# Kernel tuning notes

Hardware: AMD Instinct MI355X
Metric: run time of the kernel (lower is better)

Reference implementation:

```python
import jax, jax.numpy as jnp
import numpy as np

DIM = 4096
N_HEADS = 32
N_KV_HEADS = 8
HEAD_DIM = 128
ROPE_BASE = 10000.0
B, L = 4, 1024
NEG_INF = -1e9


def rope_traditional(x, base=ROPE_BASE, offset=0):
    # x: [B, H, L, Dh]; rotates interleaved pairs (x[...,2i], x[...,2i+1])
    Dh = x.shape[-1]
    Lx = x.shape[2]
    inv_freq = base ** (-jnp.arange(0, Dh, 2, dtype=jnp.float32) / Dh)  # [Dh/2]
    pos = jnp.arange(offset, offset + Lx, dtype=jnp.float32)
    ang = pos[:, None] * inv_freq  # [L, Dh/2]
    cos, sin = jnp.cos(ang), jnp.sin(ang)
    x1, x2 = x[..., ::2], x[..., 1::2]
    r1 = x1 * cos - x2 * sin
    r2 = x1 * sin + x2 * cos
    return jnp.stack([r1, r2], axis=-1).reshape(x.shape).astype(x.dtype)


def setup_inputs() -> dict:
    key = jax.random.key(0)
    ks = jax.random.split(key, 5)
    x = jax.random.normal(ks[0], (B, L, DIM), dtype=jnp.float32)
    # additive causal mask: 0 on/below diag, -inf-like above
    mask = jnp.where(jnp.tril(jnp.ones((L, L), dtype=bool)), 0.0, NEG_INF).astype(jnp.float32)
    wq = jax.random.normal(ks[1], (DIM, N_HEADS * HEAD_DIM), dtype=jnp.float32) * 0.02
    wk = jax.random.normal(ks[2], (DIM, N_KV_HEADS * HEAD_DIM), dtype=jnp.float32) * 0.02
    wv = jax.random.normal(ks[3], (DIM, N_KV_HEADS * HEAD_DIM), dtype=jnp.float32) * 0.02
    wo = jax.random.normal(ks[4], (N_HEADS * HEAD_DIM, DIM), dtype=jnp.float32) * 0.02
    return {"x": x, "mask": mask, "wq": wq, "wk": wk, "wv": wv, "wo": wo}


def reference(x, mask, wq, wk, wv, wo):
    Bx, Lx, D = x.shape
    scale = HEAD_DIM ** -0.5
    repeats = N_HEADS // N_KV_HEADS
    q = (x @ wq).reshape(Bx, Lx, N_HEADS, HEAD_DIM).transpose(0, 2, 1, 3)      # [B,H,L,Dh]
    k = (x @ wk).reshape(Bx, Lx, N_KV_HEADS, HEAD_DIM).transpose(0, 2, 1, 3)   # [B,Hkv,L,Dh]
    v = (x @ wv).reshape(Bx, Lx, N_KV_HEADS, HEAD_DIM).transpose(0, 2, 1, 3)
    # GQA expansion: head h attends to kv head h % n_kv_heads (matches
    # expand_dims+repeat(axis=1)+reshape in the original)
    k = jnp.tile(k, (1, repeats, 1, 1))  # [B,H,L,Dh]
    v = jnp.tile(v, (1, repeats, 1, 1))
    # cache=None path: rope with offset 0
    q = rope_traditional(q)
    k = rope_traditional(k)
    scores = jnp.einsum("bhqd,bhkd->bhqk", q * scale, k) + mask
    probs = jax.nn.softmax(scores.astype(jnp.float32), axis=-1).astype(scores.dtype)
    out = jnp.einsum("bhqk,bhkd->bhqd", probs, v)
    out = out.transpose(0, 2, 1, 3).reshape(Bx, Lx, D)
    return out @ wo
```

## Files before the change

### kernel.cpp

```cpp
#include <hip/hip_runtime.h>
#include <stdint.h>

typedef unsigned short u16;
typedef __bf16 bf16x8 __attribute__((ext_vector_type(8)));
typedef float f32x4 __attribute__((ext_vector_type(4)));

__device__ __forceinline__ u16 f2b(float x) {
  uint32_t b = __float_as_uint(x);
  b += 0x7fff + ((b >> 16) & 1);
  return (u16)(b >> 16);
}
__device__ __forceinline__ float b2f(u16 u) {
  return __uint_as_float(((uint32_t)u) << 16);
}

#define GLD16(src, dst)                                                                  \
  __builtin_amdgcn_global_load_lds((const __attribute__((address_space(1))) void*)(src),\
                                   (__attribute__((address_space(3))) void*)(dst), 16, 0, 0)

__device__ __forceinline__ f32x4 mfma16(bf16x8 a, bf16x8 b, f32x4 c) {
  return __builtin_amdgcn_mfma_f32_16x16x32_bf16(a, b, c, 0, 0, 0);
}

__global__ void k_rope_table(float2* __restrict__ tab) {
  int i = blockIdx.x * 256 + threadIdx.x;
  int l = i >> 6, d = i & 63;
  float inv = powf(10000.0f, -(float)(2 * d) / 128.0f);
  float ang = (float)l * inv;
  float s, c;
  sincosf(ang, &s, &c);
  tab[i] = make_float2(c, s);
}

__global__ void k_cast8(const float* __restrict__ src, u16* __restrict__ dst) {
  size_t i = (size_t)blockIdx.x * 256 + threadIdx.x;
  const float4* s4 = (const float4*)src;
  float4 a = s4[2 * i], b = s4[2 * i + 1];
  union { u16 u[8]; uint4 v; } o;
  o.u[0] = f2b(a.x); o.u[1] = f2b(a.y); o.u[2] = f2b(a.z); o.u[3] = f2b(a.w);
  o.u[4] = f2b(b.x); o.u[5] = f2b(b.y); o.u[6] = f2b(b.z); o.u[7] = f2b(b.w);
  ((uint4*)dst)[i] = o.v;
}

__global__ __launch_bounds__(256) void k_tcast(const float* __restrict__ src,
                                               u16* __restrict__ dst, int R, int C) {
  __shared__ u16 t[64][72];
  int tiles_c = C >> 6;
  int tr = blockIdx.x / tiles_c, tc = blockIdx.x % tiles_c;
  int tid = threadIdx.x;
  {
    int rr = tid >> 4, cv = tid & 15;
#pragma unroll
    for (int it = 0; it < 4; ++it) {
      int row = rr + it * 16;
      float4 v = *(const float4*)(src + (size_t)(tr * 64 + row) * C + tc * 64 + cv * 4);
      t[row][cv * 4 + 0] = f2b(v.x);
      t[row][cv * 4 + 1] = f2b(v.y);
      t[row][cv * 4 + 2] = f2b(v.z);
      t[row][cv * 4 + 3] = f2b(v.w);
    }
  }
  __syncthreads();
  {
    int cc = tid >> 3, g = tid & 7;
#pragma unroll
    for (int it = 0; it < 2; ++it) {
      int c = cc + it * 32;
      union { u16 u[8]; uint4 v; } o;
#pragma unroll
      for (int j = 0; j < 8; ++j) o.u[j] = t[g * 8 + j][c];
      *(uint4*)(dst + (size_t)(tc * 64 + c) * R + tr * 64 + g * 8) = o.v;
    }
  }
}

__global__ __launch_bounds__(256) void k_vtrans(const u16* __restrict__ qkv,
                                                u16* __restrict__ vrt) {
  __shared__ u16 t[64][72];
  int b = blockIdx.x >> 8;
  int tt = blockIdx.x & 255;
  int tr = tt >> 4, tc = tt & 15;
  int tid = threadIdx.x;
  {
    int rr = tid >> 3, g = tid & 7;
#pragma unroll
    for (int it = 0; it < 2; ++it) {
      int row = rr + it * 32;
      union { u16 u[8]; uint4 v; } o;
      o.v = *(const uint4*)(qkv + (size_t)(b * 1024 + tr * 64 + row) * 6144 + 5120 + tc * 64 + g * 8);
#pragma unroll
      for (int j = 0; j < 8; ++j) t[row][g * 8 + j] = o.u[j];
    }
  }
  __syncthreads();
  {
    int cc = tid >> 3, g = tid & 7;
#pragma unroll
    for (int it = 0; it < 2; ++it) {
      int c = cc + it * 32;
      union { u16 u[8]; uint4 v; } o;
#pragma unroll
      for (int j = 0; j < 8; ++j) o.u[j] = t[g * 8 + j][c];
      *(uint4*)(vrt + (size_t)(b * 1024 + tc * 64 + c) * 1024 + tr * 64 + g * 8) = o.v;
    }
  }
}

__global__ void k_rope(const u16* __restrict__ qkv, const float2* __restrict__ tab,
                       u16* __restrict__ qr, u16* __restrict__ kr) {
  int u = blockIdx.x * 256 + threadIdx.x;
  int row = u / 2560;
  int j = u - row * 2560;
  int b = row >> 10, l = row & 1023;
  const float scale = 0.08838834764831845f;
  if (j < 2048) {
    int h = j >> 6, dp = j & 63;
    uint32_t pair = *(const uint32_t*)(qkv + (size_t)row * 6144 + h * 128 + 2 * dp);
    float2 cs = tab[l * 64 + dp];
    float x1 = b2f((u16)pair), x2 = b2f((u16)(pair >> 16));
    float r1 = (x1 * cs.x - x2 * cs.y) * scale;
    float r2 = (x1 * cs.y + x2 * cs.x) * scale;
    uint32_t outw = (uint32_t)f2b(r1) | ((uint32_t)f2b(r2) << 16);
    *(uint32_t*)(qr + ((size_t)((b * 32 + h) * 1024 + l)) * 128 + 2 * dp) = outw;
  } else {
    int jj = j - 2048;
    int kh = jj >> 6, dp = jj & 63;
    uint32_t pair = *(const uint32_t*)(qkv + (size_t)row * 6144 + 4096 + kh * 128 + 2 * dp);
    float2 cs = tab[l * 64 + dp];
    float x1 = b2f((u16)pair), x2 = b2f((u16)(pair >> 16));
    float r1 = x1 * cs.x - x2 * cs.y;
    float r2 = x1 * cs.y + x2 * cs.x;
    uint32_t outw = (uint32_t)f2b(r1) | ((uint32_t)f2b(r2) << 16);
    *(uint32_t*)(kr + ((size_t)((b * 8 + kh) * 1024 + l)) * 128 + 2 * dp) = outw;
  }
}


#define LOADAB(pa, pb)                                  \
  afr[0] = *(const bf16x8*)((pa) + 0 * 512);            \
  afr[1] = *(const bf16x8*)((pa) + 1 * 512);            \
  afr[2] = *(const bf16x8*)((pa) + 2 * 512);            \
  afr[3] = *(const bf16x8*)((pa) + 3 * 512);            \
  bfr[0] = *(const bf16x8*)((pb) + 0 * 512);            \
  bfr[1] = *(const bf16x8*)((pb) + 1 * 512);            \
  bfr[2] = *(const bf16x8*)((pb) + 2 * 512);            \
  bfr[3] = *(const bf16x8*)((pb) + 3 * 512);

#define STG(kof, dA_, dB_)       \
  GLD16(sA + (kof), dA_);        \
  GLD16(sB0 + (kof), dB_);       \
  GLD16(sB1 + (kof), (dB_) + 4096);

#define MFMA16C                                                            \
  __builtin_amdgcn_s_barrier();                                            \
  asm volatile("s_waitcnt lgkmcnt(0)" ::: "memory");                       \
  __builtin_amdgcn_s_setprio(1);                                           \
  _Pragma("unroll") for (int mm = 0; mm < 4; ++mm)                         \
    _Pragma("unroll") for (int n_ = 0; n_ < 4; ++n_)                       \
      acc[mm][n_] = mfma16(afr[mm], bfr[n_], acc[mm][n_]);                 \
  __builtin_amdgcn_s_setprio(0);                                           \
  __builtin_amdgcn_s_barrier();

#define VMC(n) asm volatile("s_waitcnt vmcnt(" #n ")" ::: "memory");

template <typename OutT>
__global__ __launch_bounds__(512)
__attribute__((amdgpu_waves_per_eu(4)))
void k_gemm3(const u16* __restrict__ A,
             const u16* __restrict__ Bt,
             OutT* __restrict__ C,
             int M, int N, int K) {
  extern __shared__ u16 lds[];
  const int tid = threadIdx.x;
  const int lane = tid & 63;
  const int wid = tid >> 6;
  const int l16 = lane & 15, lhi = lane >> 4;
  const int wm = wid >> 2, wn = wid & 3;

  const int nbn = N >> 8;
  int bid = blockIdx.x;
  const int cpx = gridDim.x >> 3;
  bid = (bid & 7) * cpx + (bid >> 3);
  const int bm = (bid / nbn) << 7;
  const int bn = (bid % nbn) << 8;

  const u16* Ag = A + (size_t)bm * K;
  const u16* Bg = Bt + (size_t)bn * K;

  const int swz = (lhi ^ ((l16 >> 1) & 3)) << 3;
  const u16* pA0 = lds + wm * 2048 + l16 * 32 + swz;
  const u16* pA1 = pA0 + 4096;
  const u16* pA2 = pA0 + 8192;
  const u16* pB0 = lds + 12288 + wn * 2048 + l16 * 32 + swz;
  const u16* pB1 = pB0 + 8192;
  const u16* pB2 = pB0 + 16384;

  const int r0 = tid >> 2, g0 = tid & 3;
  const int r1 = r0 + 128;
  const size_t so0 = (size_t)r0 * K + ((g0 ^ ((r0 >> 1) & 3)) << 3);
  const size_t so1 = (size_t)r1 * K + ((g0 ^ ((r1 >> 1) & 3)) << 3);
  const u16* sA = Ag + so0;
  const u16* sB0 = Bg + so0;
  const u16* sB1 = Bg + so1;
  u16* dA0 = lds + tid * 8;
  u16* dA1 = dA0 + 4096;
  u16* dA2 = dA0 + 8192;
  u16* dB0 = lds + 12288 + tid * 8;
  u16* dB1 = dB0 + 8192;
  u16* dB2 = dB0 + 16384;

  f32x4 acc[4][4] = {};
  bf16x8 afr[4], bfr[4];

  STG(0, dA0, dB0)
  STG(32, dA1, dB1)
  VMC(3)
  __builtin_amdgcn_s_barrier();

  for (int t = 0; t < 126; t += 3) {
    const int k2 = (t + 2) * 32;
    LOADAB(pA0, pB0)
    STG(k2, dA2, dB2)
    VMC(3)
    MFMA16C
    LOADAB(pA1, pB1)
    STG(k2 + 32, dA0, dB0)
    VMC(3)
    MFMA16C
    LOADAB(pA2, pB2)
    STG(k2 + 64, dA1, dB1)
    VMC(3)
    MFMA16C
  }
  {
    LOADAB(pA0, pB0)
    VMC(0)
    MFMA16C
    LOADAB(pA1, pB1)
    MFMA16C
  }

#pragma unroll
  for (int mm = 0; mm < 4; ++mm) {
    int row = bm + wm * 64 + mm * 16 + lhi * 4;
#pragma unroll
    for (int n = 0; n < 4; ++n) {
      int col = bn + wn * 64 + n * 16 + l16;
#pragma unroll
      for (int r = 0; r < 4; ++r) {
        float v = acc[mm][n][r];
        size_t idx = (size_t)(row + r) * N + col;
        if constexpr (sizeof(OutT) == 2) C[idx] = f2b(v);
        else C[idx] = v;
      }
    }
  }
}

__global__ __launch_bounds__(512) void k_attn(const u16* __restrict__ qr,
                                              const u16* __restrict__ kr,
                                              const u16* __restrict__ vrt,
                                              u16* __restrict__ ao) {
  __shared__ u16 Klds[8192];
  __shared__ u16 Vlds[8192];
  __shared__ u16 Plds[9216];
  int bid = blockIdx.x;
  int qb = bid & 7, h = (bid >> 3) & 31, b = bid >> 8;
  int kvh = h & 7;
  int lane = threadIdx.x & 63, w = threadIdx.x >> 6;
  int l16 = lane & 15, lhi = lane >> 4;
  int qmin = qb * 128 + w * 16;

  const u16* qbase = qr + ((size_t)((b * 32 + h) * 1024) + qmin + l16) * 128;
  bf16x8 aq[4];
#pragma unroll
  for (int kc = 0; kc < 4; ++kc) aq[kc] = *(const bf16x8*)(qbase + kc * 32 + lhi * 8);

  const u16* Kg = kr + (size_t)(b * 8 + kvh) * (1024 * 128);
  const u16* Vg = vrt + (size_t)(b * 8 + kvh) * (128 * 1024);

  float m_run[4] = {-1e30f, -1e30f, -1e30f, -1e30f};
  float l_run[4] = {0.f, 0.f, 0.f, 0.f};
  f32x4 o[8] = {};

  int nkb = 2 * qb + 2;
  for (int kb = 0; kb < nkb; ++kb) {
    int kv0 = kb * 64;
#pragma unroll
    for (int i = 0; i < 2; ++i) {
      int c = w * 128 + i * 64 + lane;
      int krow = c >> 4, g = c & 15;
      GLD16(Kg + (size_t)(kv0 + krow) * 128 + ((g ^ (krow & 7)) * 8),
            Klds + (w * 128 + i * 64) * 8);
    }
#pragma unroll
    for (int i = 0; i < 2; ++i) {
      int c = w * 128 + i * 64 + lane;
      int d = c >> 3, g = c & 7;
      GLD16(Vg + (size_t)d * 1024 + kv0 + ((g ^ (d & 7)) * 8),
            Vlds + (w * 128 + i * 64) * 8);
    }
    __syncthreads();

    f32x4 s[4] = {};
#pragma unroll
    for (int kc = 0; kc < 4; ++kc) {
#pragma unroll
      for (int n = 0; n < 4; ++n) {
        int kv = n * 16 + l16;
        int g = kc * 4 + lhi;
        bf16x8 bk = *(const bf16x8*)(Klds + kv * 128 + ((g ^ (kv & 7)) * 8));
        s[n] = mfma16(aq[kc], bk, s[n]);
      }
    }
    if (kv0 + 63 > qmin) {
#pragma unroll
      for (int n = 0; n < 4; ++n)
#pragma unroll
        for (int r = 0; r < 4; ++r) {
          int q = qmin + lhi * 4 + r;
          int kv = kv0 + n * 16 + l16;
          if (kv > q) s[n][r] = -1e30f;
        }
    }
    float pr[4][4];
#pragma unroll
    for (int r = 0; r < 4; ++r) {
      float mx = fmaxf(fmaxf(s[0][r], s[1][r]), fmaxf(s[2][r], s[3][r]));
      mx = fmaxf(mx, __shfl_xor(mx, 1));
      mx = fmaxf(mx, __shfl_xor(mx, 2));
      mx = fmaxf(mx, __shfl_xor(mx, 4));
      mx = fmaxf(mx, __shfl_xor(mx, 8));
      float mn = fmaxf(m_run[r], mx);
      float sf = __expf(m_run[r] - mn);
      m_run[r] = mn;
      float sum = 0.f;
#pragma unroll
      for (int n = 0; n < 4; ++n) {
        float p = __expf(s[n][r] - mn);
        pr[n][r] = p;
        sum += p;
      }
      sum += __shfl_xor(sum, 1);
      sum += __shfl_xor(sum, 2);
      sum += __shfl_xor(sum, 4);
      sum += __shfl_xor(sum, 8);
      l_run[r] = l_run[r] * sf + sum;
#pragma unroll
      for (int nd = 0; nd < 8; ++nd) o[nd][r] *= sf;
    }
    u16* pw = Plds + w * 1152;
#pragma unroll
    for (int n = 0; n < 4; ++n)
#pragma unroll
      for (int r = 0; r < 4; ++r) pw[(lhi * 4 + r) * 72 + n * 16 + l16] = f2b(pr[n][r]);
#pragma unroll
    for (int kc = 0; kc < 2; ++kc) {
      bf16x8 ap = *(const bf16x8*)(pw + l16 * 72 + kc * 32 + lhi * 8);
#pragma unroll
      for (int nd = 0; nd < 8; ++nd) {
        int d = nd * 16 + l16;
        int g = kc * 4 + lhi;
        bf16x8 bv = *(const bf16x8*)(Vlds + d * 64 + ((g ^ (d & 7)) * 8));
        o[nd] = mfma16(ap, bv, o[nd]);
      }
    }
    __syncthreads();
  }
#pragma unroll
  for (int r = 0; r < 4; ++r) {
    float inv = 1.0f / l_run[r];
    int q = qmin + lhi * 4 + r;
    u16* orow = ao + ((size_t)(b * 1024 + q)) * 4096 + h * 128;
#pragma unroll
    for (int nd = 0; nd < 8; ++nd) orow[nd * 16 + l16] = f2b(o[nd][r] * inv);
  }
}

extern "C" void kernel_launch(void* const* d_in, const int* in_sizes, int n_in,
                              void* d_out, int out_size, void* d_ws, size_t ws_size,
                              hipStream_t stream) {
  const float* x = (const float*)d_in[0];
  const float* wq = (const float*)d_in[2];
  const float* wk = (const float*)d_in[3];
  const float* wv = (const float*)d_in[4];
  const float* wo = (const float*)d_in[5];

  char* ws = (char*)d_ws;
  u16* xb = (u16*)(ws + 0);
  u16* wcat = (u16*)(ws + 33554432);
  u16* qr = (u16*)(ws + 0);
  u16* kr = (u16*)(ws + 33554432);
  u16* vrt = (u16*)(ws + 41943040);
  u16* ao = (u16*)(ws + 50331648);
  u16* wob = (u16*)(ws + 83886080);
  float2* tab = (float2*)(ws + 117440512);
  u16* qkv = (u16*)d_out;

  hipFuncSetAttribute((const void*)k_gemm3<u16>,
                      hipFuncAttributeMaxDynamicSharedMemorySize, 73728);
  hipFuncSetAttribute((const void*)k_gemm3<float>,
                      hipFuncAttributeMaxDynamicSharedMemorySize, 73728);

  k_rope_table<<<256, 256, 0, stream>>>(tab);
  k_cast8<<<8192, 256, 0, stream>>>(x, xb);
  k_tcast<<<4096, 256, 0, stream>>>(wq, wcat, 4096, 4096);
  k_tcast<<<1024, 256, 0, stream>>>(wk, wcat + (size_t)4096 * 4096, 4096, 1024);
  k_tcast<<<1024, 256, 0, stream>>>(wv, wcat + (size_t)5120 * 4096, 4096, 1024);
  k_tcast<<<4096, 256, 0, stream>>>(wo, wob, 4096, 4096);
  k_gemm3<u16><<<768, 512, 73728, stream>>>(xb, wcat, qkv, 4096, 6144, 4096);
  k_rope<<<40960, 256, 0, stream>>>(qkv, tab, qr, kr);
  k_vtrans<<<1024, 256, 0, stream>>>(qkv, vrt);
  k_attn<<<1024, 512, 0, stream>>>(qr, kr, vrt, ao);
  k_gemm3<float><<<512, 512, 73728, stream>>>(ao, wob, (float*)d_out, 4096, 4096, 4096);
}
```

Measured before the change: 582.3 us.

## Double-buffer A fragments in registers to overlap LDS reads with MFMAs

Restructures the GEMM main loop so the next k-step's A fragments are read from LDS into a second register set while the current step's MFMAs execute. B fragments are loaded before the barrier, and the loop is unrolled by six phases with ping-pong A registers. The trip count now derives from K instead of a hardcoded constant. The goal is to hide LDS read latency behind matrix math, at the cost of extra VGPRs that could pressure occupancy under the 4-waves-per-EU setting.

```diff
diff --git a/kernel.cpp b/kernel.cpp
--- a/kernel.cpp
+++ b/kernel.cpp
@@ -136,32 +136,34 @@
 }
 
 
-#define LOADAB(pa, pb)                                  \
-  afr[0] = *(const bf16x8*)((pa) + 0 * 512);            \
-  afr[1] = *(const bf16x8*)((pa) + 1 * 512);            \
-  afr[2] = *(const bf16x8*)((pa) + 2 * 512);            \
-  afr[3] = *(const bf16x8*)((pa) + 3 * 512);            \
-  bfr[0] = *(const bf16x8*)((pb) + 0 * 512);            \
-  bfr[1] = *(const bf16x8*)((pb) + 1 * 512);            \
-  bfr[2] = *(const bf16x8*)((pb) + 2 * 512);            \
-  bfr[3] = *(const bf16x8*)((pb) + 3 * 512);
-
-#define STG(kof, dA_, dB_)       \
-  GLD16(sA + (kof), dA_);        \
-  GLD16(sB0 + (kof), dB_);       \
-  GLD16(sB1 + (kof), (dB_) + 4096);
-
-#define MFMA16C                                                            \
-  __builtin_amdgcn_s_barrier();                                            \
-  asm volatile("s_waitcnt lgkmcnt(0)" ::: "memory");                       \
-  __builtin_amdgcn_s_setprio(1);                                           \
-  _Pragma("unroll") for (int mm = 0; mm < 4; ++mm)                         \
-    _Pragma("unroll") for (int n_ = 0; n_ < 4; ++n_)                       \
-      acc[mm][n_] = mfma16(afr[mm], bfr[n_], acc[mm][n_]);                 \
-  __builtin_amdgcn_s_setprio(0);                                           \
+#define LD4(dst, base, off)                            \
+  dst[0] = *(const bf16x8*)((base) + (off) + 0 * 512); \
+  dst[1] = *(const bf16x8*)((base) + (off) + 1 * 512); \
+  dst[2] = *(const bf16x8*)((base) + (off) + 2 * 512); \
+  dst[3] = *(const bf16x8*)((base) + (off) + 3 * 512);
+
+#define STG(kof, ab, bb)                 \
+  GLD16(sA + (kof), dA + (ab));          \
+  GLD16(sB0 + (kof), dB + (bb));         \
+  GLD16(sB1 + (kof), dB + (bb) + 4096);
+
+#define VMC(n) asm volatile("s_waitcnt vmcnt(" #n ")" ::: "memory");
+
+#define MM(AF)                                             \
+  _Pragma("unroll") for (int mm = 0; mm < 4; ++mm)         \
+    _Pragma("unroll") for (int n_ = 0; n_ < 4; ++n_)       \
+      acc[mm][n_] = mfma16(AF[mm], bfr[n_], acc[mm][n_]);
+
+#define PHASE(bB, bS, bA, kof, AFc, AFn)   \
+  STG(kof, (bS) * 4096, (bS) * 8192)       \
+  VMC(3)                                   \
+  LD4(bfr, pRB, (bB) * 8192)               \
+  __builtin_amdgcn_s_barrier();            \
+  LD4(AFn, pRA, (bA) * 4096)               \
+  __builtin_amdgcn_s_setprio(1);           \
+  MM(AFc)                                  \
+  __builtin_amdgcn_s_setprio(0);           \
   __builtin_amdgcn_s_barrier();
-
-#define VMC(n) asm volatile("s_waitcnt vmcnt(" #n ")" ::: "memory");
 
 template <typename OutT>
 __global__ __launch_bounds__(512)
@@ -188,12 +190,8 @@
   const u16* Bg = Bt + (size_t)bn * K;
 
   const int swz = (lhi ^ ((l16 >> 1) & 3)) << 3;
-  const u16* pA0 = lds + wm * 2048 + l16 * 32 + swz;
-  const u16* pA1 = pA0 + 4096;
-  const u16* pA2 = pA0 + 8192;
-  const u16* pB0 = lds + 12288 + wn * 2048 + l16 * 32 + swz;
-  const u16* pB1 = pB0 + 8192;
-  const u16* pB2 = pB0 + 16384;
+  const u16* pRA = lds + wm * 2048 + l16 * 32 + swz;
+  const u16* pRB = lds + 12288 + wn * 2048 + l16 * 32 + swz;
 
   const int r0 = tid >> 2, g0 = tid & 3;
   const int r1 = r0 + 128;
@@ -202,42 +200,41 @@
   const u16* sA = Ag + so0;
   const u16* sB0 = Bg + so0;
   const u16* sB1 = Bg + so1;
-  u16* dA0 = lds + tid * 8;
-  u16* dA1 = dA0 + 4096;
-  u16* dA2 = dA0 + 8192;
-  u16* dB0 = lds + 12288 + tid * 8;
-  u16* dB1 = dB0 + 8192;
-  u16* dB2 = dB0 + 16384;
+  u16* dA = lds + tid * 8;
+  u16* dB = lds + 12288 + tid * 8;
 
   f32x4 acc[4][4] = {};
-  bf16x8 afr[4], bfr[4];
-
-  STG(0, dA0, dB0)
-  STG(32, dA1, dB1)
+  bf16x8 afrP[4], afrQ[4], bfr[4];
+
+  STG(0, 0, 0)
+  STG(32, 4096, 8192)
   VMC(3)
   __builtin_amdgcn_s_barrier();
-
-  for (int t = 0; t < 126; t += 3) {
-    const int k2 = (t + 2) * 32;
-    LOADAB(pA0, pB0)
-    STG(k2, dA2, dB2)
-    VMC(3)
-    MFMA16C
-    LOADAB(pA1, pB1)
-    STG(k2 + 32, dA0, dB0)
-    VMC(3)
-    MFMA16C
-    LOADAB(pA2, pB2)
-    STG(k2 + 64, dA1, dB1)
-    VMC(3)
-    MFMA16C
+  LD4(afrP, pRA, 0)
+
+  const int nt = K >> 5;
+  for (int t = 0; t + 6 <= nt - 2; t += 6) {
+    const int k0 = (t + 2) * 32;
+    PHASE(0, 2, 1, k0, afrP, afrQ)
+    PHASE(1, 0, 2, k0 + 32, afrQ, afrP)
+    PHASE(2, 1, 0, k0 + 64, afrP, afrQ)
+    PHASE(0, 2, 1, k0 + 96, afrQ, afrP)
+    PHASE(1, 0, 2, k0 + 128, afrP, afrQ)
+    PHASE(2, 1, 0, k0 + 160, afrQ, afrP)
   }
   {
-    LOADAB(pA0, pB0)
     VMC(0)
-    MFMA16C
-    LOADAB(pA1, pB1)
-    MFMA16C
+    LD4(bfr, pRB, 0)
+    __builtin_amdgcn_s_barrier();
+    LD4(afrQ, pRA, 4096)
+    __builtin_amdgcn_s_setprio(1);
+    MM(afrP)
+    __builtin_amdgcn_s_setprio(0);
+    __builtin_amdgcn_s_barrier();
+    LD4(bfr, pRB, 8192)
+    __builtin_amdgcn_s_setprio(1);
+    MM(afrQ)
+    __builtin_amdgcn_s_setprio(0);
   }
 
 #pragma unroll
```

Result: slower. 662.5 us (+13.8%).
